# Performance work log

Measured on AMD Instinct MI355X. Metric: run time of the kernel, lower is better.

The kernel has to match this reference:

```python
import jax, jax.numpy as jnp
import numpy as np

B, NEG = 4, 33          # queries, candidates per query
N, R = 10000, 256       # entities, relation types (even; R//2 direct)
D, L = 64, 6            # hidden dim, conv layers
E, ER = 200000, 80000   # entity edges, edges per relation graph (hh/ht/th/tt)
F = 2 * D
EPS = 1e-5


def _ln(x, s, b):
    m = jnp.mean(x, -1, keepdims=True)
    v = jnp.mean((x - m) ** 2, -1, keepdims=True)
    return (x - m) * jax.lax.rsqrt(v + EPS) * s + b


def _conv(x, boundary, relation, src, dst, etype, p):
    # GeneralizedRelationalConv (dependent=False, project_relations=True):
    # distmult message, sum aggregate + boundary self-loop, update=relu(LN(Linear([x,agg])))
    p1w, p1b, p2w, p2b, lw, lb, lns, lnb = p
    rel = jax.nn.relu(relation @ p1w + p1b) @ p2w + p2b     # relation projection MLP
    msg = x[:, src, :] * rel[:, etype, :]                   # [B, Eg, D] gathered messages
    agg = jnp.zeros_like(boundary).at[:, dst, :].add(msg) + boundary
    out = jnp.concatenate([x, agg], -1) @ lw + lb
    return jax.nn.relu(_ln(out, lns, lnb))


def _entity_bf(rel_reps, h0, r0, src, dst, etype, params):
    # NBFNet Bellman-Ford over the entity graph, query-conditioned boundary
    q = rel_reps[jnp.arange(B), r0]                         # [B, D]
    boundary = jnp.zeros((B, N, D), q.dtype).at[jnp.arange(B), h0].add(q)
    x = boundary
    for i in range(L):
        x = _conv(x, boundary, rel_reps, src, dst, etype,
                  tuple(t[i] for t in params)) + x          # short_cut residual
    nq = jnp.broadcast_to(q[:, None, :], (B, N, D))
    return jnp.concatenate([x, nq], -1)                     # [B, N, 2D]


def _forward(floats, ints):
    (e1p1w, e1p1b, e1p2w, e1p2b, e1lw, e1lb, e1lns, e1lnb,
     e2p1w, e2p1b, e2p2w, e2p2b, e2lw, e2lb, e2lns, e2lnb,
     e2m1w, e2m1b, e2m2w, e2m2b,
     rp1w, rp1b, rp2w, rp2b, rlw, rlb, rlns, rlnb, nmw, nmb) = floats
    edge_src, edge_dst, edge_type, rel_src, rel_dst, rel_etype, batch = ints
    h0 = batch[:, 0, 0]
    t_idx = batch[:, :, 1]
    r0 = batch[:, 0, 2]
    e1p = (e1p1w, e1p1b, e1p2w, e1p2b, e1lw, e1lb, e1lns, e1lnb)
    # ---- RelNet over the 4 relation graphs (nodes=relations, edge types=entities) ----
    node_reps = jnp.ones((B, N, D), e1p1w.dtype)
    q = jnp.ones((B, D), e1p1w.dtype)
    boundary = jnp.zeros((B, R, D), q.dtype).at[jnp.arange(B), r0].add(q)
    x = boundary
    for i in range(L):
        h = sum(_conv(x, boundary, node_reps, rel_src[g], rel_dst[g], rel_etype[g],
                      (rp1w[g, i], rp1b[g, i], rp2w[g, i], rp2b[g, i],
                       rlw[g, i], rlb[g, i], rlns[g, i], rlnb[g, i]))
                for g in range(4))
        x = h + x                                           # short_cut
        if i == 0:
            # entity_model_1 refreshes the per-entity (relation-graph edge type) reps
            feat = _entity_bf(x, h0, r0, edge_src, edge_dst, edge_type, e1p)
            node_reps = feat @ nmw + nmb                    # [B, N, D]
    rel_reps = x                                            # [B, R, D]
    # ---- EntityNet 2: score candidates ----
    e2p = (e2p1w, e2p1b, e2p2w, e2p2b, e2lw, e2lb, e2lns, e2lnb)
    feat2 = _entity_bf(rel_reps, h0, r0, edge_src, edge_dst, edge_type, e2p)
    g = jnp.take_along_axis(feat2, jnp.broadcast_to(t_idx[:, :, None], (B, NEG, F)), axis=1)
    score = (jax.nn.relu(g @ e2m1w + e2m1b) @ e2m2w + e2m2b)[..., 0]
    return score                                            # [B, NEG]


def setup_inputs():
    key = jax.random.key(0)
    ks = iter(jax.random.split(key, 64))
    def w(shape, std=0.08):
        return jax.random.normal(next(ks), shape, jnp.float32) * std
    inp = {}
    inp["edge_src"] = jax.random.randint(next(ks), (E,), 0, N, jnp.int32)
    inp["edge_dst"] = jax.random.randint(next(ks), (E,), 0, N, jnp.int32)
    inp["edge_type"] = jax.random.randint(next(ks), (E,), 0, R, jnp.int32)
    inp["rel_src"] = jax.random.randint(next(ks), (4, ER), 0, R, jnp.int32)
    inp["rel_dst"] = jax.random.randint(next(ks), (4, ER), 0, R, jnp.int32)
    inp["rel_etype"] = jax.random.randint(next(ks), (4, ER), 0, N, jnp.int32)
    h = jax.random.randint(next(ks), (B, 1), 0, N, jnp.int32)
    t = jax.random.randint(next(ks), (B, NEG), 0, N, jnp.int32)
    r = jax.random.randint(next(ks), (B, 1), 0, R // 2, jnp.int32)
    inp["batch"] = jnp.stack([jnp.broadcast_to(h, (B, NEG)), t,
                              jnp.broadcast_to(r, (B, NEG))], -1)
    for pre in ("e1", "e2"):
        inp[pre + "p1w"] = w((L, D, D)); inp[pre + "p1b"] = jnp.zeros((L, D))
        inp[pre + "p2w"] = w((L, D, D)); inp[pre + "p2b"] = jnp.zeros((L, D))
        inp[pre + "lw"] = w((L, F, D));  inp[pre + "lb"] = jnp.zeros((L, D))
        inp[pre + "lns"] = jnp.ones((L, D)); inp[pre + "lnb"] = jnp.zeros((L, D))
    inp["e2m1w"] = w((F, F)); inp["e2m1b"] = jnp.zeros((F,))
    inp["e2m2w"] = w((F, 1)); inp["e2m2b"] = jnp.zeros((1,))
    inp["rp1w"] = w((4, L, D, D)); inp["rp1b"] = jnp.zeros((4, L, D))
    inp["rp2w"] = w((4, L, D, D)); inp["rp2b"] = jnp.zeros((4, L, D))
    inp["rlw"] = w((4, L, F, D));  inp["rlb"] = jnp.zeros((4, L, D))
    inp["rlns"] = jnp.ones((4, L, D)); inp["rlnb"] = jnp.zeros((4, L, D))
    inp["nmw"] = w((F, D)); inp["nmb"] = jnp.zeros((D,))
    return inp


def reference(e1p1w, e1p1b, e1p2w, e1p2b, e1lw, e1lb, e1lns, e1lnb,
              e2p1w, e2p1b, e2p2w, e2p2b, e2lw, e2lb, e2lns, e2lnb,
              e2m1w, e2m1b, e2m2w, e2m2b,
              rp1w, rp1b, rp2w, rp2b, rlw, rlb, rlns, rlnb, nmw, nmb,
              edge_src, edge_dst, edge_type, rel_src, rel_dst, rel_etype, batch):
    floats = (e1p1w, e1p1b, e1p2w, e1p2b, e1lw, e1lb, e1lns, e1lnb,
              e2p1w, e2p1b, e2p2w, e2p2b, e2lw, e2lb, e2lns, e2lnb,
              e2m1w, e2m1b, e2m2w, e2m2b,
              rp1w, rp1b, rp2w, rp2b, rlw, rlb, rlns, rlnb, nmw, nmb)
    ints = (edge_src, edge_dst, edge_type, rel_src, rel_dst, rel_etype, batch)
    return _forward(floats, ints)
```

## Files before the change

### kernel.cpp

```cpp
#include <hip/hip_runtime.h>

constexpr int kB   = 4;
constexpr int kNEG = 33;
constexpr int kN   = 10000;
constexpr int kR   = 256;
constexpr int kD   = 64;
constexpr int kL   = 6;
constexpr int kE   = 200000;
constexpr int kER  = 80000;

typedef const float* fp;
typedef __attribute__((ext_vector_type(8))) short bf16x8;
typedef __attribute__((ext_vector_type(4))) float f32x4;

__device__ __forceinline__ float rdlane(float v, int l) {
  return __uint_as_float(__builtin_amdgcn_readlane(__float_as_uint(v), l));
}
__device__ __forceinline__ float wave_sum64(float v) {
  #pragma unroll
  for (int o = 32; o > 0; o >>= 1) v += __shfl_xor(v, o, 64);
  return v;
}
__device__ __forceinline__ short f2bf(float x) {
  unsigned u = __float_as_uint(x);
  unsigned r = (u + 0x7fffu + ((u >> 16) & 1u)) >> 16;
  return (short)r;
}
__device__ __forceinline__ float bf2f_u(unsigned short s) {
  return __uint_as_float(((unsigned)s) << 16);
}
__device__ __forceinline__ float bf2f(short s) { return bf2f_u((unsigned short)s); }

__global__ void k_fill(float* __restrict__ p, float v, int n) {
  int i = blockIdx.x * blockDim.x + threadIdx.x;
  int stride = gridDim.x * blockDim.x;
  for (; i < n; i += stride) p[i] = v;
}
__global__ void k_zero_i(int* __restrict__ p, int n) {
  int i = blockIdx.x * blockDim.x + threadIdx.x;
  int stride = gridDim.x * blockDim.x;
  for (; i < n; i += stride) p[i] = 0;
}
__global__ void k_add_row(float* __restrict__ dst, const int* __restrict__ batch) {
  int tid = threadIdx.x;
  int b = tid >> 6, d = tid & 63;
  int row = batch[b * kNEG * 3 + 2];
  dst[((size_t)b * kR + row) * 64 + d] += 1.0f;
}
__global__ void k_get_q(float* __restrict__ q, const float* __restrict__ relx,
                        const int* __restrict__ batch) {
  int tid = threadIdx.x;
  int b = tid >> 6, d = tid & 63;
  int r0 = batch[b * kNEG * 3 + 2];
  q[b * 64 + d] = relx[((size_t)b * kR + r0) * 64 + d];
}

__global__ void k_hist_rel_lds(const int* __restrict__ rel_dst, int* __restrict__ cnt) {
  int g = blockIdx.y;
  __shared__ int lc[256];
  lc[threadIdx.x] = 0;
  __syncthreads();
  int lo = blockIdx.x * 8000, hi = min(lo + 8000, kER);
  for (int e = lo + threadIdx.x; e < hi; e += 256)
    atomicAdd(&lc[rel_dst[(size_t)g * kER + e]], 1);
  __syncthreads();
  int c = lc[threadIdx.x];
  if (c) atomicAdd(&cnt[g * 256 + threadIdx.x], c);
}
__global__ void k_fill_rel_lds(const int* __restrict__ src, const int* __restrict__ dst,
                               const int* __restrict__ et,
                               int* __restrict__ cursor, int2* __restrict__ out) {
  int g = blockIdx.y;
  __shared__ int lc[256];
  lc[threadIdx.x] = 0;
  __syncthreads();
  int lo = blockIdx.x * 8000, hi = min(lo + 8000, kER);
  const int* db = dst + (size_t)g * kER;
  for (int e = lo + threadIdx.x; e < hi; e += 256)
    atomicAdd(&lc[db[e]], 1);
  __syncthreads();
  int c = lc[threadIdx.x];
  __syncthreads();
  lc[threadIdx.x] = c ? atomicAdd(&cursor[g * 257 + threadIdx.x], c) : 0;
  __syncthreads();
  for (int e = lo + threadIdx.x; e < hi; e += 256) {
    int bin = db[e];
    int p = atomicAdd(&lc[bin], 1);
    out[(size_t)g * kER + p] = make_int2(src[(size_t)g * kER + e], et[(size_t)g * kER + e]);
  }
}
__global__ void k_hist_ent_lds(const int* __restrict__ dst, int* __restrict__ cnt) {
  __shared__ int lc[10000];
  for (int i = threadIdx.x; i < 10000; i += 256) lc[i] = 0;
  __syncthreads();
  int lo = blockIdx.x * 12500, hi = min(lo + 12500, kE);
  for (int e = lo + threadIdx.x; e < hi; e += 256)
    atomicAdd(&lc[dst[e]], 1);
  __syncthreads();
  for (int i = threadIdx.x; i < 10000; i += 256)
    if (lc[i]) atomicAdd(&cnt[i], lc[i]);
}
__global__ void k_fill_ent_lds(const int* __restrict__ src, const int* __restrict__ dst,
                               const int* __restrict__ et,
                               int* __restrict__ cursor, int2* __restrict__ out) {
  __shared__ int lc[10000];
  for (int i = threadIdx.x; i < 10000; i += 256) lc[i] = 0;
  __syncthreads();
  int lo = blockIdx.x * 12500, hi = min(lo + 12500, kE);
  for (int e = lo + threadIdx.x; e < hi; e += 256)
    atomicAdd(&lc[dst[e]], 1);
  __syncthreads();
  for (int i = threadIdx.x; i < 10000; i += 256) {
    int c = lc[i];
    lc[i] = c ? atomicAdd(&cursor[i], c) : 0;
  }
  __syncthreads();
  for (int e = lo + threadIdx.x; e < hi; e += 256) {
    int bin = dst[e];
    int p = atomicAdd(&lc[bin], 1);
    out[p] = make_int2(src[e], et[e]);
  }
}
__global__ void k_scan_multi(const int* __restrict__ cnt, int* __restrict__ start,
                             int* __restrict__ cursor, int n, int cstride, int sstride) {
  const int* c = cnt + (size_t)blockIdx.x * cstride;
  int* st = start + (size_t)blockIdx.x * sstride;
  int* cu = cursor + (size_t)blockIdx.x * sstride;
  __shared__ int part[256];
  int t = threadIdx.x;
  int chunk = (n + 255) / 256;
  int lo = t * chunk, hi = min(lo + chunk, n);
  int s = 0;
  for (int i = lo; i < hi; ++i) s += c[i];
  part[t] = s;
  __syncthreads();
  if (t == 0) { int run = 0; for (int i = 0; i < 256; ++i) { int v = part[i]; part[i] = run; run += v; } }
  __syncthreads();
  int run = part[t];
  for (int i = lo; i < hi; ++i) { st[i] = run; cu[i] = run; run += c[i]; }
  if (t == 255) st[n] = run;
}

__global__ void k_packw(const float* __restrict__ w1, const float* __restrict__ w2,
                        short* __restrict__ w1h, short* __restrict__ w1l,
                        short* __restrict__ w2h, short* __restrict__ w2l) {
  int pg = blockIdx.x;
  for (int i = threadIdx.x; i < 4096; i += 256) {
    int t = i & 7, lane = (i >> 3) & 63, nt = (i >> 9) & 3, ks = i >> 11;
    int mr = lane & 15, kg = lane >> 4;
    int src = pg * 4096 + (ks * 32 + kg * 8 + t) * 64 + nt * 16 + mr;
    int dst = pg * 4096 + i;
    float v1 = w1[src]; short h1 = f2bf(v1);
    w1h[dst] = h1; w1l[dst] = f2bf(v1 - bf2f(h1));
    float v2 = w2[src]; short h2 = f2bf(v2);
    w2h[dst] = h2; w2l[dst] = f2bf(v2 - bf2f(h2));
  }
}

__global__ void __launch_bounds__(256) k_mlp_mfma(
    const float* __restrict__ in, const short* __restrict__ w1h, const short* __restrict__ w1l,
    const float* __restrict__ b1, const short* __restrict__ w2h, const short* __restrict__ w2l,
    const float* __restrict__ b2, int layer, unsigned short* __restrict__ out) {
  int g = blockIdx.y;
  int pg = g * kL + layer;
  int w = threadIdx.x >> 6, lane = threadIdx.x & 63;
  int mrow = lane & 15, kgrp = lane >> 4;
  int r0 = blockIdx.x * 64 + w * 16;
  __shared__ float hbuf[4][16][68];
  const float* xp = in + (size_t)(r0 + mrow) * 64 + kgrp * 8;
  bf16x8 a1h[2], a1l[2];
  #pragma unroll
  for (int ks = 0; ks < 2; ++ks) {
    #pragma unroll
    for (int t = 0; t < 8; ++t) {
      float v = xp[ks * 32 + t];
      short h = f2bf(v); a1h[ks][t] = h; a1l[ks][t] = f2bf(v - bf2f(h));
    }
  }
  const bf16x8* B1h = (const bf16x8*)(w1h + (size_t)pg * 4096);
  const bf16x8* B1l = (const bf16x8*)(w1l + (size_t)pg * 4096);
  #pragma unroll
  for (int nt = 0; nt < 4; ++nt) {
    f32x4 c = {0.f, 0.f, 0.f, 0.f};
    #pragma unroll
    for (int ks = 0; ks < 2; ++ks) {
      bf16x8 bh = B1h[(ks * 4 + nt) * 64 + lane];
      bf16x8 bl = B1l[(ks * 4 + nt) * 64 + lane];
      c = __builtin_amdgcn_mfma_f32_16x16x32_bf16(a1h[ks], bh, c, 0, 0, 0);
      c = __builtin_amdgcn_mfma_f32_16x16x32_bf16(a1h[ks], bl, c, 0, 0, 0);
      c = __builtin_amdgcn_mfma_f32_16x16x32_bf16(a1l[ks], bh, c, 0, 0, 0);
    }
    int col = nt * 16 + mrow;
    float bv = b1[pg * 64 + col];
    #pragma unroll
    for (int rg = 0; rg < 4; ++rg)
      hbuf[w][kgrp * 4 + rg][col] = fmaxf(c[rg] + bv, 0.f);
  }
  __syncthreads();
  bf16x8 a2h[2], a2l[2];
  #pragma unroll
  for (int ks = 0; ks < 2; ++ks) {
    #pragma unroll
    for (int t = 0; t < 8; ++t) {
      float v = hbuf[w][mrow][ks * 32 + kgrp * 8 + t];
      short h = f2bf(v); a2h[ks][t] = h; a2l[ks][t] = f2bf(v - bf2f(h));
    }
  }
  const bf16x8* B2h = (const bf16x8*)(w2h + (size_t)pg * 4096);
  const bf16x8* B2l = (const bf16x8*)(w2l + (size_t)pg * 4096);
  unsigned short* ob = out + (size_t)g * kB * kN * 64;
  #pragma unroll
  for (int nt = 0; nt < 4; ++nt) {
    f32x4 c = {0.f, 0.f, 0.f, 0.f};
    #pragma unroll
    for (int ks = 0; ks < 2; ++ks) {
      bf16x8 bh = B2h[(ks * 4 + nt) * 64 + lane];
      bf16x8 bl = B2l[(ks * 4 + nt) * 64 + lane];
      c = __builtin_amdgcn_mfma_f32_16x16x32_bf16(a2h[ks], bh, c, 0, 0, 0);
      c = __builtin_amdgcn_mfma_f32_16x16x32_bf16(a2h[ks], bl, c, 0, 0, 0);
      c = __builtin_amdgcn_mfma_f32_16x16x32_bf16(a2l[ks], bh, c, 0, 0, 0);
    }
    int col = nt * 16 + mrow;
    float bv = b2[pg * 64 + col];
    #pragma unroll
    for (int rg = 0; rg < 4; ++rg) {
      int grow = r0 + kgrp * 4 + rg;
      int bb = grow / kN;
      int nn = grow - bb * kN;
      ob[((size_t)nn * 4 + bb) * 64 + col] = (unsigned short)f2bf(c[rg] + bv);
    }
  }
}

__global__ void __launch_bounds__(256) k_mlp_rel6(
    const float* __restrict__ in, fp p1w, fp p1b, fp p2w, fp p2b,
    unsigned short* __restrict__ out) {
  int j = blockIdx.y;
  int row = blockIdx.x * 4 + (threadIdx.x >> 6);
  int lane = threadIdx.x & 63;
  fp W1 = p1w + (size_t)j * 4096;
  fp W2 = p2w + (size_t)j * 4096;
  float xv = in[(size_t)row * 64 + lane];
  float a = p1b[j * 64 + lane];
  float wbuf[8];
  #pragma unroll
  for (int kk = 0; kk < 64; kk += 8) {
    #pragma unroll
    for (int u = 0; u < 8; ++u) wbuf[u] = W1[(kk + u) * 64 + lane];
    #pragma unroll
    for (int u = 0; u < 8; ++u) a = fmaf(rdlane(xv, kk + u), wbuf[u], a);
  }
  a = fmaxf(a, 0.f);
  float c = p2b[j * 64 + lane];
  #pragma unroll
  for (int kk = 0; kk < 64; kk += 8) {
    #pragma unroll
    for (int u = 0; u < 8; ++u) wbuf[u] = W2[(kk + u) * 64 + lane];
    #pragma unroll
    for (int u = 0; u < 8; ++u) c = fmaf(rdlane(a, kk + u), wbuf[u], c);
  }
  int b = row >> 8, r = row & 255;
  out[(((size_t)j * kR + r) * 4 + b) * 64 + lane] = (unsigned short)f2bf(c);
}

__global__ void k_gate0(fp p1w, fp p1b, fp p2w, fp p2b, float* __restrict__ gate0) {
  int g = threadIdx.x >> 6, lane = threadIdx.x & 63;
  int pg = g * kL;
  float a = p1b[pg * 64 + lane];
  #pragma unroll
  for (int k = 0; k < 64; ++k) a += p1w[(size_t)pg * 4096 + k * 64 + lane];
  a = fmaxf(a, 0.f);
  float c = p2b[pg * 64 + lane];
  #pragma unroll
  for (int k = 0; k < 64; ++k)
    c = fmaf(rdlane(a, k), p2w[(size_t)pg * 4096 + k * 64 + lane], c);
  gate0[g * 64 + lane] = c;
}
__global__ void k_rel_agg0(const int* __restrict__ rel_start, const int2* __restrict__ rel_edges,
                           const int* __restrict__ batch, const float* __restrict__ gate0,
                           float* __restrict__ agg) {
  int wid = (blockIdx.x * blockDim.x + threadIdx.x) >> 6;
  int lane = threadIdx.x & 63;
  int g = wid >> 10, rem = wid & 1023, b = rem >> 8, r = rem & 255;
  int r0 = batch[b * kNEG * 3 + 2];
  const int* start = rel_start + g * 257;
  const int2* edges = rel_edges + (size_t)g * kER;
  int s0 = start[r], s1 = start[r + 1];
  int cnt = 0;
  for (int base = s0; base < s1; base += 64) {
    int e = base + lane;
    bool m = false;
    if (e < s1) m = (edges[e].x == r0);
    cnt += (int)__popcll(__ballot(m));
  }
  agg[(size_t)wid * 64 + lane] = gate0[g * 64 + lane] * (float)cnt + ((r == r0) ? 1.f : 0.f);
}

__global__ void __launch_bounds__(256) k_gather_rel_all(
    const float* __restrict__ rxi, const unsigned short* __restrict__ gateN,
    const int* __restrict__ rel_start, const int2* __restrict__ rel_edges,
    const int* __restrict__ batch, float* __restrict__ agg) {
  int i = blockIdx.x;
  int g = i & 3, r = i >> 2;
  const unsigned short* gate = gateN + (size_t)g * kB * kN * 64;
  const int* start = rel_start + g * 257;
  const int2* edges = rel_edges + (size_t)g * kER;
  int w = threadIdx.x >> 6, lane = threadIdx.x & 63;
  int s0 = start[r], s1 = start[r + 1];
  int len = s1 - s0;
  int per = (len + 3) >> 2;
  int e0 = s0 + w * per, e1 = min(e0 + per, s1);
  float a0 = 0.f, a1 = 0.f, a2 = 0.f, a3 = 0.f;
  int2 se;
  if (e0 < e1) se = edges[e0];
  for (int e = e0; e < e1; ++e) {
    int2 cur = se;
    if (e + 1 < e1) se = edges[e + 1];
    const float* xp = rxi + (size_t)cur.x * 256 + lane;
    const unsigned short* gp = gate + (size_t)cur.y * 256 + lane;
    a0 = fmaf(xp[0],   bf2f_u(gp[0]),   a0);
    a1 = fmaf(xp[64],  bf2f_u(gp[64]),  a1);
    a2 = fmaf(xp[128], bf2f_u(gp[128]), a2);
    a3 = fmaf(xp[192], bf2f_u(gp[192]), a3);
  }
  __shared__ float red[4][4][64];
  red[w][0][lane] = a0; red[w][1][lane] = a1; red[w][2][lane] = a2; red[w][3][lane] = a3;
  __syncthreads();
  float a = red[0][w][lane] + red[1][w][lane] + red[2][w][lane] + red[3][w][lane];
  int r0b = batch[w * kNEG * 3 + 2];
  if (r == r0b) a += 1.0f;
  agg[(((size_t)g * kB + w) * kR + r) * 64 + lane] = a;
}

__global__ void __launch_bounds__(256) k_conv_rel3(
    const float* __restrict__ rel_x, float* __restrict__ agg,
    fp rlw, fp rlb, fp rlns, fp rlnb, int layer) {
  int g = blockIdx.y;
  int pg = g * kL + layer;
  int wave = threadIdx.x >> 6, lane = threadIdx.x & 63;
  int row0 = blockIdx.x * 16 + wave * 4;
  const float* xp = rel_x + (size_t)row0 * 64 + lane;
  float* ap = agg + ((size_t)g * 1024 + row0) * 64 + lane;
  float x0 = xp[0], x1 = xp[64], x2 = xp[128], x3 = xp[192];
  float g0 = ap[0], g1 = ap[64], g2 = ap[128], g3 = ap[192];
  fp w1 = rlw + (size_t)pg * 8192;
  float bv = rlb[pg * 64 + lane];
  float o0 = bv, o1 = bv, o2 = bv, o3 = bv;
  float wbuf[8];
  #pragma unroll
  for (int kk = 0; kk < 128; kk += 8) {
    #pragma unroll
    for (int u = 0; u < 8; ++u) wbuf[u] = w1[(kk + u) * 64 + lane];
    #pragma unroll
    for (int u = 0; u < 8; ++u) {
      int k = kk + u; float w = wbuf[u];
      if (k < 64) {
        o0 = fmaf(rdlane(x0, k), w, o0); o1 = fmaf(rdlane(x1, k), w, o1);
        o2 = fmaf(rdlane(x2, k), w, o2); o3 = fmaf(rdlane(x3, k), w, o3);
      } else {
        o0 = fmaf(rdlane(g0, k - 64), w, o0); o1 = fmaf(rdlane(g1, k - 64), w, o1);
        o2 = fmaf(rdlane(g2, k - 64), w, o2); o3 = fmaf(rdlane(g3, k - 64), w, o3);
      }
    }
  }
  float s = rlns[pg * 64 + lane], t = rlnb[pg * 64 + lane];
  { float m = wave_sum64(o0) * (1.f/64.f); float c = o0 - m;
    float v = wave_sum64(c*c) * (1.f/64.f);
    ap[0] = fmaxf(c * rsqrtf(v + 1e-5f) * s + t, 0.f); }
  { float m = wave_sum64(o1) * (1.f/64.f); float c = o1 - m;
    float v = wave_sum64(c*c) * (1.f/64.f);
    ap[64] = fmaxf(c * rsqrtf(v + 1e-5f) * s + t, 0.f); }
  { float m = wave_sum64(o2) * (1.f/64.f); float c = o2 - m;
    float v = wave_sum64(c*c) * (1.f/64.f);
    ap[128] = fmaxf(c * rsqrtf(v + 1e-5f) * s + t, 0.f); }
  { float m = wave_sum64(o3) * (1.f/64.f); float c = o3 - m;
    float v = wave_sum64(c*c) * (1.f/64.f);
    ap[192] = fmaxf(c * rsqrtf(v + 1e-5f) * s + t, 0.f); }
}

__global__ void k_sum_rel(float* __restrict__ rel_x, float* __restrict__ rxi,
                          const float* __restrict__ y) {
  int i = blockIdx.x * blockDim.x + threadIdx.x;
  float v = rel_x[i] + y[i] + y[65536 + i] + y[131072 + i] + y[196608 + i];
  rel_x[i] = v;
  int d = i & 63, row = i >> 6;
  int b = row >> 8, r = row & 255;
  rxi[(((size_t)r * 4 + b) << 6) + d] = v;
}

template<bool FIRST>
__global__ void __launch_bounds__(256) k_ent_layer2(
    const float* __restrict__ xcur, float* __restrict__ xnext,
    const unsigned short* __restrict__ xbf_cur, unsigned short* __restrict__ xbf_next,
    const unsigned short* __restrict__ gateL,
    const int* __restrict__ start, const int2* __restrict__ edges,
    const float* __restrict__ q, const int* __restrict__ batch,
    fp lw, fp lb, fp lns, fp lnb) {
  int n = (blockIdx.x * blockDim.x + threadIdx.x) >> 6;
  if (n >= kN) return;
  int lane = threadIdx.x & 63;
  int h0[4]; float qv[4];
  #pragma unroll
  for (int b = 0; b < 4; ++b) { h0[b] = batch[b * kNEG * 3]; qv[b] = q[b * 64 + lane]; }
  float a0 = 0.f, a1 = 0.f, a2 = 0.f, a3 = 0.f;
  int s0 = start[n], s1 = start[n + 1];
  int2 se;
  if (s0 < s1) se = edges[s0];
  for (int e = s0; e < s1; ++e) {
    int2 cur = se;
    if (e + 1 < s1) se = edges[e + 1];
    const unsigned short* gp = gateL + (size_t)cur.y * 256 + lane;
    if (FIRST) {
      if (cur.x == h0[0]) a0 = fmaf(qv[0], bf2f_u(gp[0]),   a0);
      if (cur.x == h0[1]) a1 = fmaf(qv[1], bf2f_u(gp[64]),  a1);
      if (cur.x == h0[2]) a2 = fmaf(qv[2], bf2f_u(gp[128]), a2);
      if (cur.x == h0[3]) a3 = fmaf(qv[3], bf2f_u(gp[192]), a3);
    } else {
      const unsigned short* xp = xbf_cur + (size_t)cur.x * 256 + lane;
      a0 = fmaf(bf2f_u(xp[0]),   bf2f_u(gp[0]),   a0);
      a1 = fmaf(bf2f_u(xp[64]),  bf2f_u(gp[64]),  a1);
      a2 = fmaf(bf2f_u(xp[128]), bf2f_u(gp[128]), a2);
      a3 = fmaf(bf2f_u(xp[192]), bf2f_u(gp[192]), a3);
    }
  }
  if (n == h0[0]) a0 += qv[0];
  if (n == h0[1]) a1 += qv[1];
  if (n == h0[2]) a2 += qv[2];
  if (n == h0[3]) a3 += qv[3];
  float x0, x1, x2, x3;
  if (FIRST) {
    x0 = (n == h0[0]) ? qv[0] : 0.f; x1 = (n == h0[1]) ? qv[1] : 0.f;
    x2 = (n == h0[2]) ? qv[2] : 0.f; x3 = (n == h0[3]) ? qv[3] : 0.f;
  } else {
    const float* xp = xcur + (size_t)n * 64 + lane;
    x0 = xp[0]; x1 = xp[640000]; x2 = xp[1280000]; x3 = xp[1920000];
  }
  float bv = lb[lane];
  float o0 = bv, o1 = bv, o2 = bv, o3 = bv;
  float wbuf[8];
  #pragma unroll
  for (int kk = 0; kk < 128; kk += 8) {
    #pragma unroll
    for (int u = 0; u < 8; ++u) wbuf[u] = lw[(kk + u) * 64 + lane];
    #pragma unroll
    for (int u = 0; u < 8; ++u) {
      int k = kk + u; float w = wbuf[u];
      if (k < 64) {
        o0 = fmaf(rdlane(x0, k), w, o0); o1 = fmaf(rdlane(x1, k), w, o1);
        o2 = fmaf(rdlane(x2, k), w, o2); o3 = fmaf(rdlane(x3, k), w, o3);
      } else {
        o0 = fmaf(rdlane(a0, k - 64), w, o0); o1 = fmaf(rdlane(a1, k - 64), w, o1);
        o2 = fmaf(rdlane(a2, k - 64), w, o2); o3 = fmaf(rdlane(a3, k - 64), w, o3);
      }
    }
  }
  float s = lns[lane], t = lnb[lane];
  float* yp = xnext + (size_t)n * 64 + lane;
  unsigned short* mp = xbf_next + (size_t)n * 256 + lane;
  { float m = wave_sum64(o0) * (1.f/64.f); float c = o0 - m;
    float v = wave_sum64(c*c) * (1.f/64.f);
    float y = x0 + fmaxf(c * rsqrtf(v + 1e-5f) * s + t, 0.f);
    yp[0] = y; mp[0] = (unsigned short)f2bf(y); }
  { float m = wave_sum64(o1) * (1.f/64.f); float c = o1 - m;
    float v = wave_sum64(c*c) * (1.f/64.f);
    float y = x1 + fmaxf(c * rsqrtf(v + 1e-5f) * s + t, 0.f);
    yp[640000] = y; mp[64] = (unsigned short)f2bf(y); }
  { float m = wave_sum64(o2) * (1.f/64.f); float c = o2 - m;
    float v = wave_sum64(c*c) * (1.f/64.f);
    float y = x2 + fmaxf(c * rsqrtf(v + 1e-5f) * s + t, 0.f);
    yp[1280000] = y; mp[128] = (unsigned short)f2bf(y); }
  { float m = wave_sum64(o3) * (1.f/64.f); float c = o3 - m;
    float v = wave_sum64(c*c) * (1.f/64.f);
    float y = x3 + fmaxf(c * rsqrtf(v + 1e-5f) * s + t, 0.f);
    yp[1920000] = y; mp[192] = (unsigned short)f2bf(y); }
}

__global__ void __launch_bounds__(256) k_nodeup4(
    const float* __restrict__ x, const float* __restrict__ q,
    fp nmw, fp nmb, float* __restrict__ out) {
  int wid = (blockIdx.x * blockDim.x + threadIdx.x) >> 6;
  int lane = threadIdx.x & 63;
  int r0 = wid * 4;
  if (r0 >= kB * kN) return;
  int b = r0 / kN;
  const float* ip = x + (size_t)r0 * 64 + lane;
  float x0 = ip[0], x1 = ip[64], x2 = ip[128], x3 = ip[192];
  float qv = q[b * 64 + lane];
  float bv = nmb[lane];
  float c0 = bv, c1 = bv, c2 = bv, c3 = bv;
  float wbuf[4];
  #pragma unroll
  for (int kk = 0; kk < 64; kk += 4) {
    #pragma unroll
    for (int u = 0; u < 4; ++u) wbuf[u] = nmw[(kk + u) * 64 + lane];
    #pragma unroll
    for (int u = 0; u < 4; ++u) {
      int k = kk + u; float w = wbuf[u];
      c0 = fmaf(rdlane(x0, k), w, c0); c1 = fmaf(rdlane(x1, k), w, c1);
      c2 = fmaf(rdlane(x2, k), w, c2); c3 = fmaf(rdlane(x3, k), w, c3);
    }
  }
  float qa = 0.f;
  #pragma unroll
  for (int k = 0; k < 64; ++k)
    qa = fmaf(rdlane(qv, k), nmw[(64 + k) * 64 + lane], qa);
  float* op = out + (size_t)r0 * 64 + lane;
  op[0] = c0 + qa; op[64] = c1 + qa; op[128] = c2 + qa; op[192] = c3 + qa;
}

__global__ void k_score(const float* __restrict__ entx, const float* __restrict__ q,
                        const int* __restrict__ batch,
                        fp m1w, fp m1b, fp m2w, fp m2b,
                        float* __restrict__ out) {
  int b = blockIdx.x / kNEG, n = blockIdx.x % kNEG;
  int t = batch[(b * kNEG + n) * 3 + 1];
  int j = threadIdx.x;
  __shared__ float gv[128];
  __shared__ float red[2];
  gv[j] = (j < 64) ? entx[((size_t)b * kN + t) * 64 + j] : q[b * 64 + (j - 64)];
  __syncthreads();
  float acc = m1b[j];
  #pragma unroll 16
  for (int k = 0; k < 128; ++k)
    acc = fmaf(gv[k], m1w[k * 128 + j], acc);
  float h = fmaxf(acc, 0.f) * m2w[j];
  h = wave_sum64(h);
  if ((j & 63) == 0) red[j >> 6] = h;
  __syncthreads();
  if (j == 0) out[b * kNEG + n] = red[0] + red[1] + m2b[0];
}

extern "C" void kernel_launch(void* const* d_in, const int* in_sizes, int n_in,
                              void* d_out, int out_size, void* d_ws, size_t ws_size,
                              hipStream_t stream) {
  const int* edge_src  = (const int*)d_in[0];
  const int* edge_dst  = (const int*)d_in[1];
  const int* edge_type = (const int*)d_in[2];
  const int* rel_src   = (const int*)d_in[3];
  const int* rel_dst   = (const int*)d_in[4];
  const int* rel_etype = (const int*)d_in[5];
  const int* batch     = (const int*)d_in[6];
  fp e1p1w = (fp)d_in[7],  e1p1b = (fp)d_in[8],  e1p2w = (fp)d_in[9],  e1p2b = (fp)d_in[10];
  fp e1lw  = (fp)d_in[11], e1lb  = (fp)d_in[12], e1lns = (fp)d_in[13], e1lnb = (fp)d_in[14];
  fp e2p1w = (fp)d_in[15], e2p1b = (fp)d_in[16], e2p2w = (fp)d_in[17], e2p2b = (fp)d_in[18];
  fp e2lw  = (fp)d_in[19], e2lb  = (fp)d_in[20], e2lns = (fp)d_in[21], e2lnb = (fp)d_in[22];
  fp e2m1w = (fp)d_in[23], e2m1b = (fp)d_in[24], e2m2w = (fp)d_in[25], e2m2b = (fp)d_in[26];
  fp rp1w  = (fp)d_in[27], rp1b  = (fp)d_in[28], rp2w  = (fp)d_in[29], rp2b  = (fp)d_in[30];
  fp rlw   = (fp)d_in[31], rlb   = (fp)d_in[32], rlns  = (fp)d_in[33], rlnb  = (fp)d_in[34];
  fp nmw   = (fp)d_in[35], nmb   = (fp)d_in[36];

  float* ws = (float*)d_ws;
  float* rel_x     = ws;
  float* q         = rel_x + 65536;
  float* gate0     = q + 256;
  float* rxi       = gate0 + 256;
  float* rel_agg   = rxi + 65536;
  float* node_reps = rel_agg + 262144;
  float* ent_xa    = node_reps + 2560000;
  float* ent_xb    = ent_xa + 2560000;
  unsigned short* gateR6 = (unsigned short*)(ent_xb + 2560000);
  unsigned short* gateN  = gateR6 + 393216;
  unsigned short* ent_ba = gateN + 10240000;
  unsigned short* ent_bb = ent_ba + 2560000;
  int*   iws       = (int*)(ent_bb + 2560000);
  int2*  ent_edges = (int2*)iws;
  int2*  rel_edges = (int2*)(iws + 400000);
  int*   ent_cnt   = iws + 400000 + 640000;
  int*   ent_start = ent_cnt + 10000;
  int*   ent_cur   = ent_start + 10001;
  int*   rel_cnt   = ent_cur + 10001;
  int*   rel_start = rel_cnt + 1024;
  int*   rel_cur   = rel_start + 1028;
  short* w1hp      = (short*)(rel_cur + 1028 + 2);
  short* w1lp      = w1hp + 98304;
  short* w2hp      = w1lp + 98304;
  short* w2lp      = w2hp + 98304;

  const int nZero = 10000 + 10001 + 10001 + 1024;
  k_zero_i<<<(nZero + 255) / 256, 256, 0, stream>>>(ent_cnt, nZero);
  k_hist_ent_lds<<<16, 256, 0, stream>>>(edge_dst, ent_cnt);
  k_hist_rel_lds<<<dim3(10, 4), 256, 0, stream>>>(rel_dst, rel_cnt);
  k_scan_multi<<<1, 256, 0, stream>>>(ent_cnt, ent_start, ent_cur, 10000, 0, 0);
  k_scan_multi<<<4, 256, 0, stream>>>(rel_cnt, rel_start, rel_cur, 256, 256, 257);
  k_fill_ent_lds<<<16, 256, 0, stream>>>(edge_src, edge_dst, edge_type, ent_cur, ent_edges);
  k_fill_rel_lds<<<dim3(10, 4), 256, 0, stream>>>(rel_src, rel_dst, rel_etype, rel_cur, rel_edges);
  k_packw<<<24, 256, 0, stream>>>(rp1w, rp2w, w1hp, w1lp, w2hp, w2lp);

  k_fill<<<256, 256, 0, stream>>>(rel_x, 0.f, kB * kR * kD);
  k_add_row<<<1, 256, 0, stream>>>(rel_x, batch);

  k_gate0<<<1, 256, 0, stream>>>(rp1w, rp1b, rp2w, rp2b, gate0);
  k_rel_agg0<<<1024, 256, 0, stream>>>(rel_start, rel_edges, batch, gate0, rel_agg);
  k_conv_rel3<<<dim3(64, 4), 256, 0, stream>>>(rel_x, rel_agg, rlw, rlb, rlns, rlnb, 0);
  k_sum_rel<<<256, 256, 0, stream>>>(rel_x, rxi, rel_agg);

  k_get_q<<<1, 256, 0, stream>>>(q, rel_x, batch);
  k_mlp_rel6<<<dim3(256, 6), 256, 0, stream>>>(rel_x, e1p1w, e1p1b, e1p2w, e1p2b, gateR6);
  {
    float* cur = ent_xa; float* nxt = ent_xb;
    unsigned short* bcur = ent_ba; unsigned short* bnxt = ent_bb;
    for (int j = 0; j < kL; ++j) {
      const unsigned short* gL = gateR6 + (size_t)j * kR * 4 * 64;
      if (j == 0)
        k_ent_layer2<true><<<2500, 256, 0, stream>>>(cur, nxt, bcur, bnxt, gL, ent_start, ent_edges, q, batch,
            e1lw + (size_t)j * 8192, e1lb + (size_t)j * 64, e1lns + (size_t)j * 64, e1lnb + (size_t)j * 64);
      else
        k_ent_layer2<false><<<2500, 256, 0, stream>>>(cur, nxt, bcur, bnxt, gL, ent_start, ent_edges, q, batch,
            e1lw + (size_t)j * 8192, e1lb + (size_t)j * 64, e1lns + (size_t)j * 64, e1lnb + (size_t)j * 64);
      float* tf = cur; cur = nxt; nxt = tf;
      unsigned short* tb = bcur; bcur = bnxt; bnxt = tb;
    }
    k_nodeup4<<<2500, 256, 0, stream>>>(cur, q, nmw, nmb, node_reps);
  }

  for (int i = 1; i < kL; ++i) {
    k_mlp_mfma<<<dim3(625, 4), 256, 0, stream>>>(node_reps, w1hp, w1lp, rp1b, w2hp, w2lp, rp2b, i, gateN);
    k_gather_rel_all<<<1024, 256, 0, stream>>>(rxi, gateN, rel_start, rel_edges, batch, rel_agg);
    k_conv_rel3<<<dim3(64, 4), 256, 0, stream>>>(rel_x, rel_agg, rlw, rlb, rlns, rlnb, i);
    k_sum_rel<<<256, 256, 0, stream>>>(rel_x, rxi, rel_agg);
  }

  k_get_q<<<1, 256, 0, stream>>>(q, rel_x, batch);
  k_mlp_rel6<<<dim3(256, 6), 256, 0, stream>>>(rel_x, e2p1w, e2p1b, e2p2w, e2p2b, gateR6);
  {
    float* cur = ent_xa; float* nxt = ent_xb;
    unsigned short* bcur = ent_ba; unsigned short* bnxt = ent_bb;
    for (int j = 0; j < kL; ++j) {
      const unsigned short* gL = gateR6 + (size_t)j * kR * 4 * 64;
      if (j == 0)
        k_ent_layer2<true><<<2500, 256, 0, stream>>>(cur, nxt, bcur, bnxt, gL, ent_start, ent_edges, q, batch,
            e2lw + (size_t)j * 8192, e2lb + (size_t)j * 64, e2lns + (size_t)j * 64, e2lnb + (size_t)j * 64);
      else
        k_ent_layer2<false><<<2500, 256, 0, stream>>>(cur, nxt, bcur, bnxt, gL, ent_start, ent_edges, q, batch,
            e2lw + (size_t)j * 8192, e2lb + (size_t)j * 64, e2lns + (size_t)j * 64, e2lnb + (size_t)j * 64);
      float* tf = cur; cur = nxt; nxt = tf;
      unsigned short* tb = bcur; bcur = bnxt; bnxt = tb;
    }
    k_score<<<kB * kNEG, 128, 0, stream>>>(cur, q, batch, e2m1w, e2m1b, e2m2w, e2m2b, (float*)d_out);
  }
}
```

Baseline: 1.013 ms.

## Interleave batch dimension innermost in gathered tensors and use simple global-atomic CSR build

```diff
diff --git a/kernel.cpp b/kernel.cpp
--- a/kernel.cpp
+++ b/kernel.cpp
@@ -55,6 +55,19 @@
   q[b * 64 + d] = relx[((size_t)b * kR + r0) * 64 + d];
 }
 
+__global__ void k_hist(const int* __restrict__ dst, int ne, int* __restrict__ cnt) {
+  int i = blockIdx.x * blockDim.x + threadIdx.x;
+  if (i < ne) atomicAdd(&cnt[dst[i]], 1);
+}
+__global__ void k_fill_csr(const int* __restrict__ src, const int* __restrict__ dst,
+                           const int* __restrict__ et, int ne,
+                           int* __restrict__ cursor, int2* __restrict__ out) {
+  int i = blockIdx.x * blockDim.x + threadIdx.x;
+  if (i < ne) {
+    int p = atomicAdd(&cursor[dst[i]], 1);
+    out[p] = make_int2(src[i], et[i]);
+  }
+}
 __global__ void k_hist_rel_lds(const int* __restrict__ rel_dst, int* __restrict__ cnt) {
   int g = blockIdx.y;
   __shared__ int lc[256];
@@ -87,38 +100,6 @@
     int bin = db[e];
     int p = atomicAdd(&lc[bin], 1);
     out[(size_t)g * kER + p] = make_int2(src[(size_t)g * kER + e], et[(size_t)g * kER + e]);
-  }
-}
-__global__ void k_hist_ent_lds(const int* __restrict__ dst, int* __restrict__ cnt) {
-  __shared__ int lc[10000];
-  for (int i = threadIdx.x; i < 10000; i += 256) lc[i] = 0;
-  __syncthreads();
-  int lo = blockIdx.x * 12500, hi = min(lo + 12500, kE);
-  for (int e = lo + threadIdx.x; e < hi; e += 256)
-    atomicAdd(&lc[dst[e]], 1);
-  __syncthreads();
-  for (int i = threadIdx.x; i < 10000; i += 256)
-    if (lc[i]) atomicAdd(&cnt[i], lc[i]);
-}
-__global__ void k_fill_ent_lds(const int* __restrict__ src, const int* __restrict__ dst,
-                               const int* __restrict__ et,
-                               int* __restrict__ cursor, int2* __restrict__ out) {
-  __shared__ int lc[10000];
-  for (int i = threadIdx.x; i < 10000; i += 256) lc[i] = 0;
-  __syncthreads();
-  int lo = blockIdx.x * 12500, hi = min(lo + 12500, kE);
-  for (int e = lo + threadIdx.x; e < hi; e += 256)
-    atomicAdd(&lc[dst[e]], 1);
-  __syncthreads();
-  for (int i = threadIdx.x; i < 10000; i += 256) {
-    int c = lc[i];
-    lc[i] = c ? atomicAdd(&cursor[i], c) : 0;
-  }
-  __syncthreads();
-  for (int e = lo + threadIdx.x; e < hi; e += 256) {
-    int bin = dst[e];
-    int p = atomicAdd(&lc[bin], 1);
-    out[p] = make_int2(src[e], et[e]);
   }
 }
 __global__ void k_scan_multi(const int* __restrict__ cnt, int* __restrict__ start,
@@ -227,7 +208,7 @@
       int grow = r0 + kgrp * 4 + rg;
       int bb = grow / kN;
       int nn = grow - bb * kN;
-      ob[((size_t)nn * 4 + bb) * 64 + col] = (unsigned short)f2bf(c[rg] + bv);
+      ob[(size_t)nn * 256 + col * 4 + bb] = (unsigned short)f2bf(c[rg] + bv);
     }
   }
 }
@@ -260,7 +241,7 @@
     for (int u = 0; u < 8; ++u) c = fmaf(rdlane(a, kk + u), wbuf[u], c);
   }
   int b = row >> 8, r = row & 255;
-  out[(((size_t)j * kR + r) * 4 + b) * 64 + lane] = (unsigned short)f2bf(c);
+  out[((size_t)j * kR + r) * 256 + lane * 4 + b] = (unsigned short)f2bf(c);
 }
 
 __global__ void k_gate0(fp p1w, fp p1b, fp p2w, fp p2b, float* __restrict__ gate0) {
@@ -316,12 +297,12 @@
   for (int e = e0; e < e1; ++e) {
     int2 cur = se;
     if (e + 1 < e1) se = edges[e + 1];
-    const float* xp = rxi + (size_t)cur.x * 256 + lane;
-    const unsigned short* gp = gate + (size_t)cur.y * 256 + lane;
-    a0 = fmaf(xp[0],   bf2f_u(gp[0]),   a0);
-    a1 = fmaf(xp[64],  bf2f_u(gp[64]),  a1);
-    a2 = fmaf(xp[128], bf2f_u(gp[128]), a2);
-    a3 = fmaf(xp[192], bf2f_u(gp[192]), a3);
+    float4 xv4 = *((const float4*)(rxi + (size_t)cur.x * 256) + lane);
+    ushort4 gv4 = *((const ushort4*)(gate + (size_t)cur.y * 256) + lane);
+    a0 = fmaf(xv4.x, bf2f_u(gv4.x), a0);
+    a1 = fmaf(xv4.y, bf2f_u(gv4.y), a1);
+    a2 = fmaf(xv4.z, bf2f_u(gv4.z), a2);
+    a3 = fmaf(xv4.w, bf2f_u(gv4.w), a3);
   }
   __shared__ float red[4][4][64];
   red[w][0][lane] = a0; red[w][1][lane] = a1; red[w][2][lane] = a2; red[w][3][lane] = a3;
@@ -385,7 +366,7 @@
   rel_x[i] = v;
   int d = i & 63, row = i >> 6;
   int b = row >> 8, r = row & 255;
-  rxi[(((size_t)r * 4 + b) << 6) + d] = v;
+  rxi[(size_t)r * 256 + d * 4 + b] = v;
 }
 
 template<bool FIRST>
@@ -409,18 +390,18 @@
   for (int e = s0; e < s1; ++e) {
     int2 cur = se;
     if (e + 1 < s1) se = edges[e + 1];
-    const unsigned short* gp = gateL + (size_t)cur.y * 256 + lane;
+    ushort4 gv4 = *((const ushort4*)(gateL + (size_t)cur.y * 256) + lane);
     if (FIRST) {
-      if (cur.x == h0[0]) a0 = fmaf(qv[0], bf2f_u(gp[0]),   a0);
-      if (cur.x == h0[1]) a1 = fmaf(qv[1], bf2f_u(gp[64]),  a1);
-      if (cur.x == h0[2]) a2 = fmaf(qv[2], bf2f_u(gp[128]), a2);
-      if (cur.x == h0[3]) a3 = fmaf(qv[3], bf2f_u(gp[192]), a3);
+      if (cur.x == h0[0]) a0 = fmaf(qv[0], bf2f_u(gv4.x), a0);
+      if (cur.x == h0[1]) a1 = fmaf(qv[1], bf2f_u(gv4.y), a1);
+      if (cur.x == h0[2]) a2 = fmaf(qv[2], bf2f_u(gv4.z), a2);
+      if (cur.x == h0[3]) a3 = fmaf(qv[3], bf2f_u(gv4.w), a3);
     } else {
-      const unsigned short* xp = xbf_cur + (size_t)cur.x * 256 + lane;
-      a0 = fmaf(bf2f_u(xp[0]),   bf2f_u(gp[0]),   a0);
-      a1 = fmaf(bf2f_u(xp[64]),  bf2f_u(gp[64]),  a1);
-      a2 = fmaf(bf2f_u(xp[128]), bf2f_u(gp[128]), a2);
-      a3 = fmaf(bf2f_u(xp[192]), bf2f_u(gp[192]), a3);
+      ushort4 xv4 = *((const ushort4*)(xbf_cur + (size_t)cur.x * 256) + lane);
+      a0 = fmaf(bf2f_u(xv4.x), bf2f_u(gv4.x), a0);
+      a1 = fmaf(bf2f_u(xv4.y), bf2f_u(gv4.y), a1);
+      a2 = fmaf(bf2f_u(xv4.z), bf2f_u(gv4.z), a2);
+      a3 = fmaf(bf2f_u(xv4.w), bf2f_u(gv4.w), a3);
     }
   }
   if (n == h0[0]) a0 += qv[0];
@@ -456,23 +437,23 @@
   }
   float s = lns[lane], t = lnb[lane];
   float* yp = xnext + (size_t)n * 64 + lane;
-  unsigned short* mp = xbf_next + (size_t)n * 256 + lane;
+  float y0, y1, y2, y3;
   { float m = wave_sum64(o0) * (1.f/64.f); float c = o0 - m;
     float v = wave_sum64(c*c) * (1.f/64.f);
-    float y = x0 + fmaxf(c * rsqrtf(v + 1e-5f) * s + t, 0.f);
-    yp[0] = y; mp[0] = (unsigned short)f2bf(y); }
+    y0 = x0 + fmaxf(c * rsqrtf(v + 1e-5f) * s + t, 0.f); yp[0] = y0; }
   { float m = wave_sum64(o1) * (1.f/64.f); float c = o1 - m;
     float v = wave_sum64(c*c) * (1.f/64.f);
-    float y = x1 + fmaxf(c * rsqrtf(v + 1e-5f) * s + t, 0.f);
-    yp[640000] = y; mp[64] = (unsigned short)f2bf(y); }
+    y1 = x1 + fmaxf(c * rsqrtf(v + 1e-5f) * s + t, 0.f); yp[640000] = y1; }
   { float m = wave_sum64(o2) * (1.f/64.f); float c = o2 - m;
     float v = wave_sum64(c*c) * (1.f/64.f);
-    float y = x2 + fmaxf(c * rsqrtf(v + 1e-5f) * s + t, 0.f);
-    yp[1280000] = y; mp[128] = (unsigned short)f2bf(y); }
+    y2 = x2 + fmaxf(c * rsqrtf(v + 1e-5f) * s + t, 0.f); yp[1280000] = y2; }
   { float m = wave_sum64(o3) * (1.f/64.f); float c = o3 - m;
     float v = wave_sum64(c*c) * (1.f/64.f);
-    float y = x3 + fmaxf(c * rsqrtf(v + 1e-5f) * s + t, 0.f);
-    yp[1920000] = y; mp[192] = (unsigned short)f2bf(y); }
+    y3 = x3 + fmaxf(c * rsqrtf(v + 1e-5f) * s + t, 0.f); yp[1920000] = y3; }
+  ushort4 m4;
+  m4.x = (unsigned short)f2bf(y0); m4.y = (unsigned short)f2bf(y1);
+  m4.z = (unsigned short)f2bf(y2); m4.w = (unsigned short)f2bf(y3);
+  *((ushort4*)(xbf_next + (size_t)n * 256) + lane) = m4;
 }
 
 __global__ void __launch_bounds__(256) k_nodeup4(
@@ -578,11 +559,11 @@
 
   const int nZero = 10000 + 10001 + 10001 + 1024;
   k_zero_i<<<(nZero + 255) / 256, 256, 0, stream>>>(ent_cnt, nZero);
-  k_hist_ent_lds<<<16, 256, 0, stream>>>(edge_dst, ent_cnt);
+  k_hist<<<(kE + 255) / 256, 256, 0, stream>>>(edge_dst, kE, ent_cnt);
   k_hist_rel_lds<<<dim3(10, 4), 256, 0, stream>>>(rel_dst, rel_cnt);
   k_scan_multi<<<1, 256, 0, stream>>>(ent_cnt, ent_start, ent_cur, 10000, 0, 0);
   k_scan_multi<<<4, 256, 0, stream>>>(rel_cnt, rel_start, rel_cur, 256, 256, 257);
-  k_fill_ent_lds<<<16, 256, 0, stream>>>(edge_src, edge_dst, edge_type, ent_cur, ent_edges);
+  k_fill_csr<<<(kE + 255) / 256, 256, 0, stream>>>(edge_src, edge_dst, edge_type, kE, ent_cur, ent_edges);
   k_fill_rel_lds<<<dim3(10, 4), 256, 0, stream>>>(rel_src, rel_dst, rel_etype, rel_cur, rel_edges);
   k_packw<<<24, 256, 0, stream>>>(rp1w, rp2w, w1hp, w1lp, w2hp, w2lp);
 
@@ -600,7 +581,7 @@
     float* cur = ent_xa; float* nxt = ent_xb;
     unsigned short* bcur = ent_ba; unsigned short* bnxt = ent_bb;
     for (int j = 0; j < kL; ++j) {
-      const unsigned short* gL = gateR6 + (size_t)j * kR * 4 * 64;
+      const unsigned short* gL = gateR6 + (size_t)j * kR * 256;
       if (j == 0)
         k_ent_layer2<true><<<2500, 256, 0, stream>>>(cur, nxt, bcur, bnxt, gL, ent_start, ent_edges, q, batch,
             e1lw + (size_t)j * 8192, e1lb + (size_t)j * 64, e1lns + (size_t)j * 64, e1lnb + (size_t)j * 64);
@@ -626,7 +607,7 @@
     float* cur = ent_xa; float* nxt = ent_xb;
     unsigned short* bcur = ent_ba; unsigned short* bnxt = ent_bb;
     for (int j = 0; j < kL; ++j) {
-      const unsigned short* gL = gateR6 + (size_t)j * kR * 4 * 64;
+      const unsigned short* gL = gateR6 + (size_t)j * kR * 256;
       if (j == 0)
         k_ent_layer2<true><<<2500, 256, 0, stream>>>(cur, nxt, bcur, bnxt, gL, ent_start, ent_edges, q, batch,
             e2lw + (size_t)j * 8192, e2lb + (size_t)j * 64, e2lns + (size_t)j * 64, e2lnb + (size_t)j * 64);
```

After: 1.011 ms. No clear change (-0.3%).
